# Kernel optimization log

Hardware: AMD Instinct MI355X
Metric: run time of the kernel (lower is better)

The kernel has to match this reference:

```python
import jax, jax.numpy as jnp
import numpy as np

B, S, D, F_, E, K = 64, 8, 2048, 4096, 8, 2


def setup_inputs() -> dict:
    key = jax.random.key(0)
    ks = jax.random.split(key, 5)
    scale_in = 1.0 / np.sqrt(D)
    scale_ff = 1.0 / np.sqrt(F_)
    return {
        "x": jax.random.normal(ks[0], (B, S, D), dtype=jnp.float32),
        "gate_w": jax.random.normal(ks[1], (D, E), dtype=jnp.float32) * scale_in,
        "w1": jax.random.normal(ks[2], (E, D, F_), dtype=jnp.float32) * scale_in,
        "w3": jax.random.normal(ks[3], (E, D, F_), dtype=jnp.float32) * scale_in,
        "w2": jax.random.normal(ks[4], (E, F_, D), dtype=jnp.float32) * scale_ff,
        "top_k": K,
    }


def reference(x, gate_w, w1, w3, w2, top_k):
    # x: [B,S,D]; gate_w: [D,E]; w1,w3: [E,D,F]; w2: [E,F,D]
    n_experts = gate_w.shape[-1]
    gate_logits = jnp.einsum("bsd,de->bse", x, gate_w)          # [B,S,E]
    weights, selected = jax.lax.top_k(gate_logits, top_k)        # [B,S,K]
    weights = jax.nn.softmax(weights, axis=-1)                   # softmax over k (dim=2)
    # per-token combine weight for every expert: [B,S,E]
    combine = jnp.einsum(
        "bsk,bske->bse", weights, jax.nn.one_hot(selected, n_experts, dtype=x.dtype)
    )
    # SwiGLU expert FFN, batched over the (small, fixed) expert axis
    h = jax.nn.silu(jnp.einsum("bsd,edf->ebsf", x, w1)) * jnp.einsum(
        "bsd,edf->ebsf", x, w3
    )                                                            # [E,B,S,F]
    expert_out = jnp.einsum("ebsf,efd->ebsd", h, w2)             # [E,B,S,D]
    return jnp.einsum("bse,ebsd->bsd", combine, expert_out)      # [B,S,D]
```

## Files before the change

kernel.cpp:

```cpp
#include <hip/hip_runtime.h>
#include <hip/hip_bf16.h>
#include <cstdint>
#include <cstddef>

#define NB   64
#define NS   8
#define DIM  2048
#define FF   4096
#define NE   8
#define TOK  512
#define NPAIR 1024

#define BM   192
#define BKE  32
#define ASZ  (BM * 4 * 8)

typedef __attribute__((ext_vector_type(4))) float f32x4;
typedef __attribute__((ext_vector_type(8))) short bf16x8;

#define MFMA16(a, b, c) __builtin_amdgcn_mfma_f32_16x16x32_bf16((a), (b), (c), 0, 0, 0)
#define SCHEDBAR __builtin_amdgcn_sched_barrier(0)
#define LGKMBAR do { asm volatile("s_waitcnt lgkmcnt(0)" ::: "memory"); \
                     asm volatile("s_barrier" ::: "memory");            \
                     __builtin_amdgcn_sched_barrier(0); } while (0)

static __device__ __forceinline__ short f2bf(float f) {
    unsigned u = __builtin_bit_cast(unsigned, f);
    return (short)((u + 0x8000u) >> 16);
}
static __device__ __forceinline__ unsigned cvtpk(float lo, float hi) {
    unsigned r;
    asm("v_cvt_pk_bf16_f32 %0, %1, %2" : "=v"(r) : "v"(lo), "v"(hi));
    return r;
}
static __device__ __forceinline__ bf16x8 pack8(const float* v) {
    uint4 u;
    u.x = cvtpk(v[0], v[1]); u.y = cvtpk(v[2], v[3]);
    u.z = cvtpk(v[4], v[5]); u.w = cvtpk(v[6], v[7]);
    return __builtin_bit_cast(bf16x8, u);
}

static __device__ __forceinline__ void async16(void* l, const void* g) {
    __builtin_amdgcn_global_load_lds(
        (const __attribute__((address_space(1))) void*)g,
        (__attribute__((address_space(3))) void*)l, 16, 0, 0);
}

__global__ void gate_topk(const float* __restrict__ x, const float* __restrict__ gw,
                          unsigned short* __restrict__ xbf,
                          int* __restrict__ tok_expert, float* __restrict__ tok_gatew) {
    int token = blockIdx.x;
    int lane  = threadIdx.x;
    const float* xr = x + (size_t)token * DIM;

    float acc[NE];
#pragma unroll
    for (int e = 0; e < NE; ++e) acc[e] = 0.f;

    for (int d0 = lane * 8; d0 < DIM; d0 += 64 * 8) {
        float4 xa = *(const float4*)(xr + d0);
        float4 xb = *(const float4*)(xr + d0 + 4);
        bf16x8 v;
        v[0] = f2bf(xa.x); v[1] = f2bf(xa.y); v[2] = f2bf(xa.z); v[3] = f2bf(xa.w);
        v[4] = f2bf(xb.x); v[5] = f2bf(xb.y); v[6] = f2bf(xb.z); v[7] = f2bf(xb.w);
        *(bf16x8*)(xbf + (size_t)token * DIM + d0) = v;
#pragma unroll
        for (int j = 0; j < 8; ++j) {
            float xv = (j < 4) ? ((const float*)&xa)[j] : ((const float*)&xb)[j - 4];
            const float4* g = (const float4*)(gw + (size_t)(d0 + j) * NE);
            float4 g0 = g[0], g1 = g[1];
            acc[0] += xv * g0.x; acc[1] += xv * g0.y;
            acc[2] += xv * g0.z; acc[3] += xv * g0.w;
            acc[4] += xv * g1.x; acc[5] += xv * g1.y;
            acc[6] += xv * g1.z; acc[7] += xv * g1.w;
        }
    }
#pragma unroll
    for (int off = 32; off >= 1; off >>= 1) {
#pragma unroll
        for (int e = 0; e < NE; ++e) acc[e] += __shfl_down(acc[e], off);
    }
    if (lane == 0) {
        float b1 = -1e30f, b2 = -1e30f; int i1 = 0, i2 = 0;
#pragma unroll
        for (int e = 0; e < NE; ++e) {
            float v = acc[e];
            if (v > b1) { b2 = b1; i2 = i1; b1 = v; i1 = e; }
            else if (v > b2) { b2 = v; i2 = e; }
        }
        float t = __expf(b2 - b1);
        tok_expert[token * 2 + 0] = i1;
        tok_expert[token * 2 + 1] = i2;
        tok_gatew[token * 2 + 0] = 1.f / (1.f + t);
        tok_gatew[token * 2 + 1] = t / (1.f + t);
    }
}

__global__ void build_lists(const int* __restrict__ tok_expert,
                            const float* __restrict__ tok_gatew,
                            int* __restrict__ counts, int* __restrict__ offsets,
                            int* __restrict__ row_token, float* __restrict__ row_gatew,
                            int* __restrict__ pair_row) {
    __shared__ int s_off[NE];
    __shared__ int s_cnt[NE];
    int e    = threadIdx.x >> 6;
    int lane = threadIdx.x & 63;
    unsigned long long lt = (1ull << lane) - 1ull;

    int cnt = 0;
    for (int base = 0; base < NPAIR; base += 64) {
        int id = tok_expert[base + lane];
        unsigned long long m = __ballot(id == e);
        cnt += __popcll(m);
    }
    if (lane == 0) s_cnt[e] = cnt;
    __syncthreads();
    if (threadIdx.x == 0) {
        int o = 0;
        for (int i = 0; i < NE; ++i) {
            int c = s_cnt[i];
            counts[i] = c; offsets[i] = o; s_off[i] = o; o += c;
        }
    }
    __syncthreads();

    int rbase = s_off[e];
    for (int base = 0; base < NPAIR; base += 64) {
        int entry = base + lane;
        int id = tok_expert[entry];
        bool match = (id == e);
        unsigned long long m = __ballot(match);
        int pre = __popcll(m & lt);
        if (match) {
            int row = rbase + pre;
            row_token[row] = entry >> 1;
            row_gatew[row] = tok_gatew[entry];
            pair_row[entry] = row;
        }
        rbase += __popcll(m);
    }
}

#define EP1(RD, WR, BSR, BSW, PACKV, LOADV, S, HAS_P, HAS_W) do {           \
    if (HAS_P) {                                                            \
        if (t < 768) async16(&(WR)[(size_t)t * 8], asrc0 + ((S) + 2) * BKE);\
    }                                                                       \
    SCHEDBAR;                                                               \
    if (HAS_P) {                                                            \
        _Pragma("unroll")                                                   \
        for (int j = 0; j < 8; ++j)                                         \
            LOADV[j] = bsrc[(size_t)(((S) + 2) * BKE + j) * FF];            \
    }                                                                       \
    SCHEDBAR;                                                               \
    bf16x8 a_[3];                                                           \
    _Pragma("unroll")                                                       \
    for (int f = 0; f < 3; ++f) {                                           \
        int r_ = wm * 48 + f * 16 + l15;                                    \
        int p_ = (lg + (r_ >> 1)) & 3;                                      \
        a_[f] = *(const bf16x8*)&(RD)[((size_t)r_ * 4 + p_) * 8];           \
    }                                                                       \
    _Pragma("unroll")                                                       \
    for (int nf = 0; nf < 2; ++nf) {                                        \
        int ch_ = wn * 32 + nf * 16 + l15 + lg * 128;                       \
        bf16x8 b1f = *(const bf16x8*)&Bs[BSR][0][ch_][0];                   \
        bf16x8 b3f = *(const bf16x8*)&Bs[BSR][1][ch_][0];                   \
        _Pragma("unroll")                                                   \
        for (int f = 0; f < 3; ++f) {                                       \
            acc1[f][nf] = MFMA16(a_[f], b1f, acc1[f][nf]);                  \
            acc3[f][nf] = MFMA16(a_[f], b3f, acc3[f][nf]);                  \
        }                                                                   \
    }                                                                       \
    if (HAS_W) {                                                            \
        bf16x8 wv = pack8(PACKV);                                           \
        *(bf16x8*)&Bs[BSW][bmat][bch][0] = wv;                              \
    }                                                                       \
    LGKMBAR;                                                                \
} while (0)

__global__ __launch_bounds__(1024, 4) void ffn1(
    const unsigned short* __restrict__ xbf, const float* __restrict__ w1,
    const float* __restrict__ w3,
    const int* __restrict__ counts, const int* __restrict__ offsets,
    const int* __restrict__ row_token, unsigned short* __restrict__ Hbuf) {
    __shared__ __align__(16) unsigned short As[3 * ASZ];
    __shared__ __align__(16) unsigned short Bs[2][2][512][8];

    int bid = blockIdx.x;
    int e  = bid & 7;
    int f0 = (bid >> 3) * 128;

    int Me = counts[e];
    if (Me == 0) return;
    int off = offsets[e];

    int t = threadIdx.x;
    int lane = t & 63;
    int w = t >> 6;
    int wm = w >> 2, wn = w & 3;
    int l15 = lane & 15, lg = lane >> 4;

    const float* w1e = w1 + (size_t)e * DIM * FF + f0;
    const float* w3e = w3 + (size_t)e * DIM * FF + f0;

    int bmat = t >> 9;
    int bc   = t & 511;
    int bcol = bc & 127, blg = bc >> 7;
    const float* bsrc = (bmat ? w3e : w1e) + (size_t)(blg * 8) * FF + bcol;
    int bch = bcol + blg * 128;

    const int NST = DIM / BKE;

    for (int mb = 0; mb < Me; mb += BM) {
        __syncthreads();
        const unsigned short* asrc0 = xbf;
        {
            int m0 = t >> 2, c0 = t & 3;
            int rl0 = mb + m0;
            int tok0 = row_token[off + ((rl0 < Me) ? rl0 : (Me - 1))];
            asrc0 = xbf + (size_t)tok0 * DIM + (((c0 - (m0 >> 1)) & 3) << 3);
        }

        f32x4 acc1[3][2], acc3[3][2];
#pragma unroll
        for (int f = 0; f < 3; ++f)
#pragma unroll
            for (int nf = 0; nf < 2; ++nf) {
                acc1[f][nf] = (f32x4){0.f, 0.f, 0.f, 0.f};
                acc3[f][nf] = (f32x4){0.f, 0.f, 0.f, 0.f};
            }

        unsigned short* pRd = As;
        unsigned short* pMd = As + ASZ;
        unsigned short* pWr = As + 2 * ASZ;

        float bX[8], bY[8];

        if (t < 768) {
            async16(&pRd[(size_t)t * 8], asrc0);
            async16(&pMd[(size_t)t * 8], asrc0 + BKE);
        }
        SCHEDBAR;
#pragma unroll
        for (int j = 0; j < 8; ++j) bX[j] = bsrc[(size_t)j * FF];
        {
            bf16x8 wv = pack8(bX);
            *(bf16x8*)&Bs[0][bmat][bch][0] = wv;
        }
#pragma unroll
        for (int j = 0; j < 8; ++j) bY[j] = bsrc[(size_t)(BKE + j) * FF];
        LGKMBAR;

        for (int s = 0; s < NST - 2; s += 2) {
            EP1(pRd, pWr, 0, 1, bY, bX, s,     1, 1);
            EP1(pMd, pRd, 1, 0, bX, bY, s + 1, 1, 1);
            unsigned short* tt = pRd; pRd = pWr; pWr = pMd; pMd = tt;
        }
        EP1(pRd, pWr, 0, 1, bY, bX, NST - 2, 0, 1);
        EP1(pMd, pRd, 1, 0, bX, bY, NST - 1, 0, 0);

#pragma unroll
        for (int f = 0; f < 3; ++f)
#pragma unroll
            for (int nf = 0; nf < 2; ++nf)
#pragma unroll
                for (int r = 0; r < 4; ++r) {
                    int rl = mb + wm * 48 + f * 16 + lg * 4 + r;
                    if (rl < Me) {
                        float a1 = acc1[f][nf][r], a3 = acc3[f][nf][r];
                        float h = (a1 / (1.f + __expf(-a1))) * a3;
                        Hbuf[(size_t)(off + rl) * FF + f0 + wn * 32 + nf * 16 + l15] =
                            (unsigned short)f2bf(h);
                    }
                }
    }
}

#define EP2(RD, WR, BSR, BSW, PACKV, LOADV, S, HAS_P, HAS_W) do {           \
    if (HAS_P) {                                                            \
        async16(&(WR)[(size_t)t * 8], asrc0 + ((S) + 2) * BKE);             \
        if (t < 256)                                                        \
            async16(&(WR)[(size_t)(512 + t) * 8], asrc1 + ((S) + 2) * BKE); \
    }                                                                       \
    SCHEDBAR;                                                               \
    if (HAS_P) {                                                            \
        _Pragma("unroll")                                                   \
        for (int j = 0; j < 4; ++j)                                         \
            LOADV[j] = bsrc[(size_t)(((S) + 2) * BKE + j) * DIM];           \
    }                                                                       \
    SCHEDBAR;                                                               \
    bf16x8 a_[3];                                                           \
    _Pragma("unroll")                                                       \
    for (int f = 0; f < 3; ++f) {                                           \
        int r_ = wm * 48 + f * 16 + l15;                                    \
        int p_ = (lg + (r_ >> 1)) & 3;                                      \
        a_[f] = *(const bf16x8*)&(RD)[((size_t)r_ * 4 + p_) * 8];           \
    }                                                                       \
    _Pragma("unroll")                                                       \
    for (int nf = 0; nf < 2; ++nf) {                                        \
        int ch_ = wn * 32 + nf * 16 + l15 + lg * 64;                        \
        bf16x8 bw = *(const bf16x8*)&Bs[BSR][ch_][0];                       \
        _Pragma("unroll")                                                   \
        for (int f = 0; f < 3; ++f)                                         \
            acc[f][nf] = MFMA16(a_[f], bw, acc[f][nf]);                     \
    }                                                                       \
    if (HAS_W) {                                                            \
        uint2 u_;                                                           \
        u_.x = cvtpk(PACKV[0], PACKV[1]);                                   \
        u_.y = cvtpk(PACKV[2], PACKV[3]);                                   \
        *(uint2*)&Bs[BSW][bch][bhalf * 4] = u_;                             \
    }                                                                       \
    LGKMBAR;                                                                \
} while (0)

__global__ __launch_bounds__(512, 4) void ffn2(
    const unsigned short* __restrict__ Hbuf, const float* __restrict__ w2,
    const int* __restrict__ counts, const int* __restrict__ offsets,
    const float* __restrict__ row_gatew, float* __restrict__ OP) {
    __shared__ __align__(16) unsigned short As[3 * ASZ];
    __shared__ __align__(16) unsigned short Bs[2][256][8];

    int bid = blockIdx.x;
    int e  = bid & 7;
    int d0 = (bid >> 3) * 64;

    int Me = counts[e];
    if (Me == 0) return;
    int off = offsets[e];

    int t = threadIdx.x;
    int lane = t & 63;
    int w = t >> 6;
    int wm = w >> 1, wn = w & 1;
    int l15 = lane & 15, lg = lane >> 4;

    const float* w2e = w2 + (size_t)e * FF * DIM + d0;

    int bcol = t & 63, blg = (t >> 6) & 3, bhalf = t >> 8;
    const float* bsrc = w2e + (size_t)(blg * 8 + bhalf * 4) * DIM + bcol;
    int bch = bcol + blg * 64;

    const int NST = FF / BKE;

    for (int mb = 0; mb < Me; mb += BM) {
        __syncthreads();
        const unsigned short* asrc0;
        const unsigned short* asrc1;
        {
            int m0 = t >> 2, c0 = t & 3;
            int rl0 = mb + m0;
            asrc0 = Hbuf + (size_t)(off + ((rl0 < Me) ? rl0 : (Me - 1))) * FF
                         + (((c0 - (m0 >> 1)) & 3) << 3);
            int i1 = 512 + t;
            int m1 = i1 >> 2, c1 = i1 & 3;
            int rl1 = mb + m1;
            asrc1 = Hbuf + (size_t)(off + ((rl1 < Me) ? rl1 : (Me - 1))) * FF
                         + (((c1 - (m1 >> 1)) & 3) << 3);
        }

        f32x4 acc[3][2];
#pragma unroll
        for (int f = 0; f < 3; ++f)
#pragma unroll
            for (int nf = 0; nf < 2; ++nf) acc[f][nf] = (f32x4){0.f, 0.f, 0.f, 0.f};

        unsigned short* pRd = As;
        unsigned short* pMd = As + ASZ;
        unsigned short* pWr = As + 2 * ASZ;

        float bX[4], bY[4];

        async16(&pRd[(size_t)t * 8], asrc0);
        if (t < 256) async16(&pRd[(size_t)(512 + t) * 8], asrc1);
        async16(&pMd[(size_t)t * 8], asrc0 + BKE);
        if (t < 256) async16(&pMd[(size_t)(512 + t) * 8], asrc1 + BKE);
        SCHEDBAR;
#pragma unroll
        for (int j = 0; j < 4; ++j) bX[j] = bsrc[(size_t)j * DIM];
        {
            uint2 u_;
            u_.x = cvtpk(bX[0], bX[1]);
            u_.y = cvtpk(bX[2], bX[3]);
            *(uint2*)&Bs[0][bch][bhalf * 4] = u_;
        }
#pragma unroll
        for (int j = 0; j < 4; ++j) bY[j] = bsrc[(size_t)(BKE + j) * DIM];
        LGKMBAR;

        for (int s = 0; s < NST - 2; s += 2) {
            EP2(pRd, pWr, 0, 1, bY, bX, s,     1, 1);
            EP2(pMd, pRd, 1, 0, bX, bY, s + 1, 1, 1);
            unsigned short* tt = pRd; pRd = pWr; pWr = pMd; pMd = tt;
        }
        EP2(pRd, pWr, 0, 1, bY, bX, NST - 2, 0, 1);
        EP2(pMd, pRd, 1, 0, bX, bY, NST - 1, 0, 0);

#pragma unroll
        for (int f = 0; f < 3; ++f)
#pragma unroll
            for (int nf = 0; nf < 2; ++nf)
#pragma unroll
                for (int r = 0; r < 4; ++r) {
                    int rl = mb + wm * 48 + f * 16 + lg * 4 + r;
                    if (rl < Me) {
                        int grow = off + rl;
                        float g = row_gatew[grow];
                        OP[(size_t)grow * DIM + d0 + wn * 32 + nf * 16 + l15] =
                            acc[f][nf][r] * g;
                    }
                }
    }
}

__global__ void combine(const float* __restrict__ OP, const int* __restrict__ pair_row,
                        float* __restrict__ out) {
    int idx = blockIdx.x * blockDim.x + threadIdx.x;
    int token = idx >> 9;
    int q = idx & 511;
    int r0 = pair_row[token * 2 + 0];
    int r1 = pair_row[token * 2 + 1];
    float4 a = *(const float4*)(OP + (size_t)r0 * DIM + q * 4);
    float4 b = *(const float4*)(OP + (size_t)r1 * DIM + q * 4);
    float4 o;
    o.x = a.x + b.x; o.y = a.y + b.y; o.z = a.z + b.z; o.w = a.w + b.w;
    *(float4*)(out + (size_t)token * DIM + q * 4) = o;
}

extern "C" void kernel_launch(void* const* d_in, const int* in_sizes, int n_in,
                              void* d_out, int out_size, void* d_ws, size_t ws_size,
                              hipStream_t stream) {
    const float* x  = (const float*)d_in[0];
    const float* gw = (const float*)d_in[1];
    const float* w1 = (const float*)d_in[2];
    const float* w3 = (const float*)d_in[3];
    const float* w2 = (const float*)d_in[4];
    float* out = (float*)d_out;

    char* ws = (char*)d_ws;
    unsigned short* Hbuf = (unsigned short*)ws;
    float* OP            = (float*)(ws + 8388608);
    unsigned short* xbf  = (unsigned short*)(ws + 16777216);
    char* meta           = ws + 18874368;
    int*   tok_expert = (int*)(meta);
    float* tok_gatew  = (float*)(meta + 4096);
    int*   counts     = (int*)(meta + 8192);
    int*   offsets    = (int*)(meta + 8224);
    int*   row_token  = (int*)(meta + 8256);
    float* row_gatew  = (float*)(meta + 12352);
    int*   pair_row   = (int*)(meta + 16448);

    gate_topk<<<TOK, 64, 0, stream>>>(x, gw, xbf, tok_expert, tok_gatew);
    build_lists<<<1, 512, 0, stream>>>(tok_expert, tok_gatew, counts, offsets,
                                       row_token, row_gatew, pair_row);
    ffn1<<<NE * 32, 1024, 0, stream>>>(xbf, w1, w3, counts, offsets, row_token, Hbuf);
    ffn2<<<NE * 32, 512, 0, stream>>>(Hbuf, w2, counts, offsets, row_gatew, OP);
    combine<<<1024, 256, 0, stream>>>(OP, pair_row, out);
}
```

Before: 210.9 us.

## Split ffn2 reduction dimension in two and sum partials in combine

The down-projection kernel now splits the F reduction into two halves, launching twice as many blocks. Each half writes its partial result to a separate workspace buffer, and the combine kernel adds both partials for both expert rows. This raises parallelism for the ffn2 stage, where 256 blocks under-fill the GPU. The cost is an extra partial buffer and twice the combine read traffic.

```diff
diff --git a/kernel.cpp b/kernel.cpp
--- a/kernel.cpp
+++ b/kernel.cpp
@@ -315,13 +315,18 @@
 __global__ __launch_bounds__(512, 4) void ffn2(
     const unsigned short* __restrict__ Hbuf, const float* __restrict__ w2,
     const int* __restrict__ counts, const int* __restrict__ offsets,
-    const float* __restrict__ row_gatew, float* __restrict__ OP) {
+    const float* __restrict__ row_gatew,
+    float* __restrict__ OPa, float* __restrict__ OPb) {
     __shared__ __align__(16) unsigned short As[3 * ASZ];
     __shared__ __align__(16) unsigned short Bs[2][256][8];
 
     int bid = blockIdx.x;
-    int e  = bid & 7;
-    int d0 = (bid >> 3) * 64;
+    int e   = bid & 7;
+    int idx = bid >> 3;
+    int d0 = (idx >> 1) * 64;
+    int ks = idx & 1;
+    int k0 = ks * (FF / 2);
+    float* OP = ks ? OPb : OPa;
 
     int Me = counts[e];
     if (Me == 0) return;
@@ -336,10 +341,10 @@
     const float* w2e = w2 + (size_t)e * FF * DIM + d0;
 
     int bcol = t & 63, blg = (t >> 6) & 3, bhalf = t >> 8;
-    const float* bsrc = w2e + (size_t)(blg * 8 + bhalf * 4) * DIM + bcol;
+    const float* bsrc = w2e + (size_t)(k0 + blg * 8 + bhalf * 4) * DIM + bcol;
     int bch = bcol + blg * 64;
 
-    const int NST = FF / BKE;
+    const int NST = (FF / 2) / BKE;
 
     for (int mb = 0; mb < Me; mb += BM) {
         __syncthreads();
@@ -349,12 +354,12 @@
             int m0 = t >> 2, c0 = t & 3;
             int rl0 = mb + m0;
             asrc0 = Hbuf + (size_t)(off + ((rl0 < Me) ? rl0 : (Me - 1))) * FF
-                         + (((c0 - (m0 >> 1)) & 3) << 3);
+                         + k0 + (((c0 - (m0 >> 1)) & 3) << 3);
             int i1 = 512 + t;
             int m1 = i1 >> 2, c1 = i1 & 3;
             int rl1 = mb + m1;
             asrc1 = Hbuf + (size_t)(off + ((rl1 < Me) ? rl1 : (Me - 1))) * FF
-                         + (((c1 - (m1 >> 1)) & 3) << 3);
+                         + k0 + (((c1 - (m1 >> 1)) & 3) << 3);
         }
 
         f32x4 acc[3][2];
@@ -411,17 +416,22 @@
     }
 }
 
-__global__ void combine(const float* __restrict__ OP, const int* __restrict__ pair_row,
-                        float* __restrict__ out) {
+__global__ void combine(const float* __restrict__ OPa, const float* __restrict__ OPb,
+                        const int* __restrict__ pair_row, float* __restrict__ out) {
     int idx = blockIdx.x * blockDim.x + threadIdx.x;
     int token = idx >> 9;
     int q = idx & 511;
     int r0 = pair_row[token * 2 + 0];
     int r1 = pair_row[token * 2 + 1];
-    float4 a = *(const float4*)(OP + (size_t)r0 * DIM + q * 4);
-    float4 b = *(const float4*)(OP + (size_t)r1 * DIM + q * 4);
+    float4 a0 = *(const float4*)(OPa + (size_t)r0 * DIM + q * 4);
+    float4 b0 = *(const float4*)(OPb + (size_t)r0 * DIM + q * 4);
+    float4 a1 = *(const float4*)(OPa + (size_t)r1 * DIM + q * 4);
+    float4 b1 = *(const float4*)(OPb + (size_t)r1 * DIM + q * 4);
     float4 o;
-    o.x = a.x + b.x; o.y = a.y + b.y; o.z = a.z + b.z; o.w = a.w + b.w;
+    o.x = (a0.x + b0.x) + (a1.x + b1.x);
+    o.y = (a0.y + b0.y) + (a1.y + b1.y);
+    o.z = (a0.z + b0.z) + (a1.z + b1.z);
+    o.w = (a0.w + b0.w) + (a1.w + b1.w);
     *(float4*)(out + (size_t)token * DIM + q * 4) = o;
 }
 
@@ -437,9 +447,10 @@
 
     char* ws = (char*)d_ws;
     unsigned short* Hbuf = (unsigned short*)ws;
-    float* OP            = (float*)(ws + 8388608);
+    float* OPa           = (float*)(ws + 8388608);
     unsigned short* xbf  = (unsigned short*)(ws + 16777216);
-    char* meta           = ws + 18874368;
+    float* OPb           = (float*)(ws + 20971520);
+    char* meta           = ws + 29360128;
     int*   tok_expert = (int*)(meta);
     float* tok_gatew  = (float*)(meta + 4096);
     int*   counts     = (int*)(meta + 8192);
@@ -452,6 +463,6 @@
     build_lists<<<1, 512, 0, stream>>>(tok_expert, tok_gatew, counts, offsets,
                                        row_token, row_gatew, pair_row);
     ffn1<<<NE * 32, 1024, 0, stream>>>(xbf, w1, w3, counts, offsets, row_token, Hbuf);
-    ffn2<<<NE * 32, 512, 0, stream>>>(Hbuf, w2, counts, offsets, row_gatew, OP);
-    combine<<<1024, 256, 0, stream>>>(OP, pair_row, out);
-}
+    ffn2<<<NE * 64, 512, 0, stream>>>(Hbuf, w2, counts, offsets, row_gatew, OPa, OPb);
+    combine<<<1024, 256, 0, stream>>>(OPa, OPb, pair_row, out);
+}
```

Result: faster. 198.4 us (median of 2 runs) (-5.9%).
